# Kernel tuning notes

Measured on AMD Instinct MI355X. Metric: run time of the kernel, lower is better.

Reference implementation:

```python
import jax, jax.numpy as jnp
import numpy as np

N = 256          # batch size
C = 100          # nb_classes
D = 512          # sz_embed
SCALE = 3.0
EPS = 1e-12      # F.normalize eps
M = N * (N - 1) // 2  # number of (i<j) candidate pairs


def l2norm(x):
    # matches F.normalize(p=2, dim=-1) with eps=1e-12
    return x / jnp.maximum(jnp.linalg.norm(x, axis=-1, keepdims=True), EPS)


def dist_block(A, B):
    # squared euclidean distance block of pairwise_distance(cat([A,B]))[0][:len(A), len(A):]
    # (off-diagonal block, so the eye-masking in the original is a no-op; negatives zeroed)
    d = (A * A).sum(-1, keepdims=True) + (B * B).sum(-1)[None, :] - 2.0 * (A @ B.T)
    return jnp.maximum(d, 0.0)


def setup_inputs() -> dict:
    key = jax.random.key(0)
    k1, k2, k3 = jax.random.split(key, 3)
    X = jax.random.normal(k1, (N, D), dtype=jnp.float32)
    proxies = jax.random.normal(k2, (C, D), dtype=jnp.float32) / 8.0
    T = jax.random.randint(k3, (N,), 0, C)
    indices = jnp.arange(N)  # unused by forward, kept for signature fidelity
    return {"X": X, "proxies": proxies, "T": T, "indices": indices}


def reference(X, proxies, T, indices):
    Pn = SCALE * l2norm(proxies)           # (C, D)
    Xn = SCALE * l2norm(X)                 # (N, D)
    IP = Xn @ Pn.T                         # (N, C) inner-product block

    # --- intercls_mixup (method=1, uncertainty-guided lambdas) ---
    # all i<j pairs; same-class pairs are masked out (original skips them in a Python loop)
    i1, i2 = jnp.triu_indices(N, k=1)      # (M,), (M,)
    diff = T[i1] != T[i2]                  # (M,) valid cross-class pairs
    c1, c2 = T[i1], T[i2]

    X1P1 = jnp.clip(IP[i1, c1], -1.0, 1.0)
    X1P2 = jnp.clip(IP[i1, c2], -1.0, 1.0)
    X2P1 = jnp.clip(IP[i2, c1], -1.0, 1.0)
    X2P2 = jnp.clip(IP[i2, c2], -1.0, 1.0)
    lam = jnp.clip((X2P2 - X2P1) / (X2P2 - X2P1 + X1P1 - X1P2), 0.3, 0.7)
    lam = jnp.where(diff, lam, 0.5)        # neutralize masked (same-class) pairs

    virt = lam[:, None] * Xn[i1] + (1.0 - lam[:, None]) * Xn[i2]  # (M, D)
    virt = l2norm(virt)

    # --- proxy-NCA loss over real + virtual samples ---
    Xall = jnp.concatenate([Xn, SCALE * virt], axis=0)            # (N+M, D)
    Dall = dist_block(Xall, Pn)                                   # (N+M, C)
    logsm = jax.nn.log_softmax(-Dall, axis=-1)

    loss_real = -logsm[jnp.arange(N), T]                          # one-hot targets
    lv = logsm[N:]                                                # (M, C)
    rows = jnp.arange(M)
    # virtual soft targets: lam*onehot(c1) + (1-lam)*onehot(c2)
    loss_virt = -(lam * lv[rows, c1] + (1.0 - lam) * lv[rows, c2])

    total = loss_real.sum() + jnp.sum(jnp.where(diff, loss_virt, 0.0))
    count = N + diff.sum()
    return total / count
```

## Files before the change

kernel.cpp:

```cpp
#include <hip/hip_runtime.h>
#include <hip/hip_bf16.h>
#include <math.h>

#define N_ 256
#define C_ 100
#define D_ 512
#define ST 368
#define NTILE 23
#define NWTILE 529
#define LOG2E 1.44269504088896f

typedef __attribute__((ext_vector_type(8))) short short8;
typedef __attribute__((ext_vector_type(4))) float floatx4;

__device__ inline float waveReduceSum(float v) {
    #pragma unroll
    for (int off = 32; off > 0; off >>= 1) v += __shfl_xor(v, off, 64);
    return v;
}
__device__ inline float clip1(float x) { return fminf(fmaxf(x, -1.0f), 1.0f); }

__device__ inline short8 cvt8(float4 a, float4 b) {
    union { __hip_bfloat16 h[8]; short8 s; } u;
    u.h[0] = __float2bfloat16(a.x); u.h[1] = __float2bfloat16(a.y);
    u.h[2] = __float2bfloat16(a.z); u.h[3] = __float2bfloat16(a.w);
    u.h[4] = __float2bfloat16(b.x); u.h[5] = __float2bfloat16(b.y);
    u.h[6] = __float2bfloat16(b.z); u.h[7] = __float2bfloat16(b.w);
    return u.s;
}

__global__ void gemm_kernel(const float* __restrict__ X,
                            const float* __restrict__ P,
                            float* __restrict__ G,
                            float* __restrict__ rn) {
    int wid = blockIdx.x * 4 + (threadIdx.x >> 6);
    if (wid >= NWTILE) return;
    int lane = threadIdx.x & 63;
    int r = lane & 15, quad = lane >> 4;
    int tm = wid / NTILE, tn = wid - tm * NTILE;
    int ra = tm * 16 + r; if (ra >= 356) ra = 0;
    int rb = tn * 16 + r; if (rb >= 356) rb = 0;
    const float* arow = (ra < N_) ? (X + (size_t)ra * D_) : (P + (size_t)(ra - N_) * D_);
    const float* brow = (rb < N_) ? (X + (size_t)rb * D_) : (P + (size_t)(rb - N_) * D_);
    floatx4 acc = {0.0f, 0.0f, 0.0f, 0.0f};
    #pragma unroll
    for (int kc = 0; kc < D_; kc += 32) {
        const float4* ap = (const float4*)(arow + kc + quad * 8);
        const float4* bp = (const float4*)(brow + kc + quad * 8);
        short8 av = cvt8(ap[0], ap[1]);
        short8 bv = cvt8(bp[0], bp[1]);
        acc = __builtin_amdgcn_mfma_f32_16x16x32_bf16(av, bv, acc, 0, 0, 0);
    }
    int row0 = tm * 16 + quad * 4, col = tn * 16 + r;
    #pragma unroll
    for (int i = 0; i < 4; ++i)
        G[(size_t)(row0 + i) * ST + col] = acc[i];
    if (tm == tn && (r >> 2) == quad) {
        float d = acc[r & 3];
        rn[tm * 16 + r] = 3.0f * rsqrtf(fmaxf(d, 1e-24f));
    }
}

__global__ __launch_bounds__(512)
void pair_kernel(const float* __restrict__ G, const float* __restrict__ rn,
                 const int* __restrict__ T, float* __restrict__ out) {
    __shared__ __attribute__((aligned(16))) float XPl[64 * 104];
    __shared__ __attribute__((aligned(16))) float al[104];
    __shared__ __attribute__((aligned(16))) float sps[104];
    __shared__ float gl[256];
    __shared__ float sxs[256];
    __shared__ int   Tl[256];
    __shared__ int   hist[104];
    __shared__ float red[8];

    int t = threadIdx.x;
    int w = t >> 6, lane = t & 63;
    int bh = blockIdx.x;
    int b = bh & 255, h = bh >> 8;
    int base = h * 64 + 1;

    if (t < 104) { hist[t] = 0; sps[t] = (t < C_) ? rn[256 + t] : 0.0f; }
    if (t < 256) { sxs[t] = rn[t]; Tl[t] = T[t]; gl[t] = G[(size_t)b * ST + t]; }
    if (t < C_)  al[t] = G[(size_t)b * ST + 256 + t];
    #pragma unroll
    for (int it = 0; it < 4; ++it) {
        int id = t + 512 * it;
        if (id < 1600) {
            int row = id / 25, c4 = id - row * 25;
            int gr = (b + base + row) & 255;
            *(float4*)&XPl[row * 104 + c4 * 4] =
                *(const float4*)(G + (size_t)gr * ST + 256 + c4 * 4);
        }
    }
    __syncthreads();
    if (t < 256) atomicAdd(&hist[Tl[t]], 1);

    int m = t >> 3, q = t & 7;
    int t1 = Tl[b];
    float s1 = sxs[b];
    float contrib = 0.0f;
    int nit = (h == 0 && m == 0) ? 2 : 1;
    for (int it = 0; it < nit; ++it) {
        bool isdiag = (it == 1);
        int dd = base + m;
        int i2 = isdiag ? b : ((b + dd) & 255);
        int t2 = Tl[i2];
        bool act = isdiag || ((t2 != t1) && (dd < 128 || b < 128));
        if (!act) continue;
        const float* rowB = isdiag ? al : &XPl[m * 104];
        float sc2 = sxs[i2];
        float ip11 = al[t1] * s1 * sps[t1];
        float ip12 = al[t2] * s1 * sps[t2];
        float ip21 = rowB[t1] * sc2 * sps[t1];
        float ip22 = rowB[t2] * sc2 * sps[t2];
        float X1P1 = clip1(ip11), X1P2 = clip1(ip12);
        float X2P1 = clip1(ip21), X2P2 = clip1(ip22);
        float num = X2P2 - X2P1;
        float den = num + X1P1 - X1P2;
        float lam = fminf(fmaxf(num / den, 0.3f), 0.7f);
        if (isdiag) lam = 1.0f;
        float oml = 1.0f - lam;
        float g = gl[i2] * s1 * sc2;
        float wn2 = 9.0f * (lam * lam + oml * oml) + 2.0f * lam * oml * g;
        float ss2 = 6.0f * rsqrtf(fmaxf(wn2, 1e-24f));
        float la = ss2 * lam * s1 * LOG2E, lb = ss2 * oml * sc2 * LOG2E;
        float sm = 0.0f;
        #pragma unroll
        for (int k = 0; k < 4; ++k) {
            int c = q * 4 + 32 * k;
            if (c < C_) {
                float4 a1 = *(const float4*)&al[c];
                float4 a2 = *(const float4*)&rowB[c];
                float4 s4 = *(const float4*)&sps[c];
                sm += exp2f(s4.x * (la * a1.x + lb * a2.x));
                sm += exp2f(s4.y * (la * a1.y + lb * a2.y));
                sm += exp2f(s4.z * (la * a1.z + lb * a2.z));
                sm += exp2f(s4.w * (la * a1.w + lb * a2.w));
            }
        }
        sm += __shfl_xor(sm, 1, 64);
        sm += __shfl_xor(sm, 2, 64);
        sm += __shfl_xor(sm, 4, 64);
        if (q == 0) {
            float LSE = logf(sm);
            float ec1 = ss2 * (lam * ip11 + oml * ip21);
            float ec2 = ss2 * (lam * ip12 + oml * ip22);
            contrib += LSE - lam * ec1 - oml * ec2;
        }
    }
    float rsum = waveReduceSum(contrib);
    if (lane == 0) red[w] = rsum;
    __syncthreads();

    if (w == 0) {
        float same = 0.0f;
        { float n = (float)hist[lane]; same = 0.5f * n * (n - 1.0f); }
        if (lane + 64 < C_) { float n = (float)hist[lane + 64]; same += 0.5f * n * (n - 1.0f); }
        float bs = (lane < 8) ? red[lane] : 0.0f;
        same = waveReduceSum(same);
        bs = waveReduceSum(bs);
        if (lane == 0) atomicAdd(out, bs / (32896.0f - same));
    }
}

extern "C" void kernel_launch(void* const* d_in, const int* in_sizes, int n_in,
                              void* d_out, int out_size, void* d_ws, size_t ws_size,
                              hipStream_t stream) {
    const float* X = (const float*)d_in[0];
    const float* P = (const float*)d_in[1];
    const int*   T = (const int*)d_in[2];
    float* ws = (float*)d_ws;
    float* G  = ws;
    float* rn = ws + 135424;
    float* out = (float*)d_out;

    gemm_kernel<<<133, 256, 0, stream>>>(X, P, G, rn);
    pair_kernel<<<512, 512, 0, stream>>>(G, rn, T, out);
}
```

Baseline: 77.54 us.

## Split GEMM into X·X, X·P, P·P tiles with K-split and transposed IP layout

The gram GEMM now computes only the needed tiles: X·Xᵀ, X·Pᵀ stored in a class-chunk-major float4 layout, and only the diagonal of P·Pᵀ. Each tile's K dimension is split across four waves and reduced through shared memory. The pair kernel uses one 1024-thread block per row b, with 4 lanes per pair reading the inner-product rows straight from global memory instead of staging them in LDS. This removes redundant P·P and X·P tile work, raises GEMM parallelism and drops the LDS staging. In exchange, the pair kernel takes uncoalesced-ish global reads and has wave imbalance because only j>b pairs are active.

```diff
diff --git a/kernel.cpp b/kernel.cpp
--- a/kernel.cpp
+++ b/kernel.cpp
@@ -5,10 +5,11 @@
 #define N_ 256
 #define C_ 100
 #define D_ 512
-#define ST 368
-#define NTILE 23
-#define NWTILE 529
 #define LOG2E 1.44269504088896f
+
+#define WS_GX  0
+#define WS_GTP 65536
+#define WS_RN  91136
 
 typedef __attribute__((ext_vector_type(8))) short short8;
 typedef __attribute__((ext_vector_type(4))) float floatx4;
@@ -29,134 +30,147 @@
     return u.s;
 }
 
-__global__ void gemm_kernel(const float* __restrict__ X,
-                            const float* __restrict__ P,
-                            float* __restrict__ G,
-                            float* __restrict__ rn) {
-    int wid = blockIdx.x * 4 + (threadIdx.x >> 6);
-    if (wid >= NWTILE) return;
-    int lane = threadIdx.x & 63;
+__global__ __launch_bounds__(256)
+void gemm_kernel(const float* __restrict__ X, const float* __restrict__ P,
+                 float* __restrict__ ws) {
+    float* Gx  = ws + WS_GX;
+    float* GTP = ws + WS_GTP;
+    float* rn  = ws + WS_RN;
+    __shared__ floatx4 accl[3][64];
+    int tile = blockIdx.x;
+    int t = threadIdx.x, w = t >> 6, lane = t & 63;
     int r = lane & 15, quad = lane >> 4;
-    int tm = wid / NTILE, tn = wid - tm * NTILE;
-    int ra = tm * 16 + r; if (ra >= 356) ra = 0;
-    int rb = tn * 16 + r; if (rb >= 356) rb = 0;
-    const float* arow = (ra < N_) ? (X + (size_t)ra * D_) : (P + (size_t)(ra - N_) * D_);
-    const float* brow = (rb < N_) ? (X + (size_t)rb * D_) : (P + (size_t)(rb - N_) * D_);
+    const float *arow, *brow;
+    int tm, tn, mode;
+    if (tile < 256) {
+        mode = 0; tm = tile >> 4; tn = tile & 15;
+        arow = X + (size_t)(tm * 16 + r) * D_;
+        brow = X + (size_t)(tn * 16 + r) * D_;
+    } else if (tile < 368) {
+        int u = tile - 256; mode = 1; tm = u / 7; tn = u - tm * 7;
+        int pb = tn * 16 + r; if (pb >= C_) pb = 0;
+        arow = X + (size_t)(tm * 16 + r) * D_;
+        brow = P + (size_t)pb * D_;
+    } else {
+        mode = 2; tm = tile - 368; tn = tm;
+        int pa = tm * 16 + r; if (pa >= C_) pa = 0;
+        arow = P + (size_t)pa * D_;
+        brow = arow;
+    }
     floatx4 acc = {0.0f, 0.0f, 0.0f, 0.0f};
+    int k0 = w * 128;
     #pragma unroll
-    for (int kc = 0; kc < D_; kc += 32) {
-        const float4* ap = (const float4*)(arow + kc + quad * 8);
-        const float4* bp = (const float4*)(brow + kc + quad * 8);
+    for (int kk = 0; kk < 128; kk += 32) {
+        const float4* ap = (const float4*)(arow + k0 + kk + quad * 8);
+        const float4* bp = (const float4*)(brow + k0 + kk + quad * 8);
         short8 av = cvt8(ap[0], ap[1]);
         short8 bv = cvt8(bp[0], bp[1]);
         acc = __builtin_amdgcn_mfma_f32_16x16x32_bf16(av, bv, acc, 0, 0, 0);
     }
-    int row0 = tm * 16 + quad * 4, col = tn * 16 + r;
-    #pragma unroll
-    for (int i = 0; i < 4; ++i)
-        G[(size_t)(row0 + i) * ST + col] = acc[i];
-    if (tm == tn && (r >> 2) == quad) {
-        float d = acc[r & 3];
-        rn[tm * 16 + r] = 3.0f * rsqrtf(fmaxf(d, 1e-24f));
+    if (w) accl[w - 1][lane] = acc;
+    __syncthreads();
+    if (w == 0) {
+        acc += accl[0][lane]; acc += accl[1][lane]; acc += accl[2][lane];
+        if (mode == 0) {
+            int row0 = tm * 16 + quad * 4, col = tn * 16 + r;
+            #pragma unroll
+            for (int i = 0; i < 4; ++i) Gx[(row0 + i) * 256 + col] = acc[i];
+            if (tm == tn && (r >> 2) == quad)
+                rn[tm * 16 + r] = 3.0f * rsqrtf(fmaxf(acc[r & 3], 1e-24f));
+        } else if (mode == 1) {
+            int c = tn * 16 + r;
+            if (c < C_) {
+                int row0 = tm * 16 + quad * 4;
+                #pragma unroll
+                for (int i = 0; i < 4; ++i)
+                    GTP[(c >> 2) * 1024 + (row0 + i) * 4 + (c & 3)] = acc[i];
+            }
+        } else {
+            if ((r >> 2) == quad) {
+                int pr = tm * 16 + r;
+                if (pr < C_) rn[256 + pr] = 3.0f * rsqrtf(fmaxf(acc[r & 3], 1e-24f));
+            }
+        }
     }
 }
 
-__global__ __launch_bounds__(512)
-void pair_kernel(const float* __restrict__ G, const float* __restrict__ rn,
-                 const int* __restrict__ T, float* __restrict__ out) {
-    __shared__ __attribute__((aligned(16))) float XPl[64 * 104];
-    __shared__ __attribute__((aligned(16))) float al[104];
-    __shared__ __attribute__((aligned(16))) float sps[104];
-    __shared__ float gl[256];
-    __shared__ float sxs[256];
-    __shared__ int   Tl[256];
-    __shared__ int   hist[104];
-    __shared__ float red[8];
+__global__ __launch_bounds__(1024)
+void pair_kernel(const float* __restrict__ ws, const int* __restrict__ T,
+                 float* __restrict__ out) {
+    const float* Gx  = ws + WS_GX;
+    const float4* G4 = (const float4*)(ws + WS_GTP);
+    const float* rn  = ws + WS_RN;
+    __shared__ int Tl[256];
+    __shared__ int hist[C_];
+    __shared__ float sxl[256];
+    __shared__ float red[16];
 
-    int t = threadIdx.x;
-    int w = t >> 6, lane = t & 63;
-    int bh = blockIdx.x;
-    int b = bh & 255, h = bh >> 8;
-    int base = h * 64 + 1;
-
-    if (t < 104) { hist[t] = 0; sps[t] = (t < C_) ? rn[256 + t] : 0.0f; }
-    if (t < 256) { sxs[t] = rn[t]; Tl[t] = T[t]; gl[t] = G[(size_t)b * ST + t]; }
-    if (t < C_)  al[t] = G[(size_t)b * ST + 256 + t];
-    #pragma unroll
-    for (int it = 0; it < 4; ++it) {
-        int id = t + 512 * it;
-        if (id < 1600) {
-            int row = id / 25, c4 = id - row * 25;
-            int gr = (b + base + row) & 255;
-            *(float4*)&XPl[row * 104 + c4 * 4] =
-                *(const float4*)(G + (size_t)gr * ST + 256 + c4 * 4);
-        }
-    }
+    int t = threadIdx.x, w = t >> 6, lane = t & 63;
+    int b = blockIdx.x;
+    if (t < 256) { Tl[t] = T[t]; sxl[t] = rn[t]; }
+    if (t < C_) hist[t] = 0;
     __syncthreads();
     if (t < 256) atomicAdd(&hist[Tl[t]], 1);
 
-    int m = t >> 3, q = t & 7;
+    int m = t >> 2, p = t & 3;
     int t1 = Tl[b];
-    float s1 = sxs[b];
+    float s1 = sxl[b];
+    bool diag = (m == b);
+    bool act = diag || ((m > b) && (Tl[m] != t1));
     float contrib = 0.0f;
-    int nit = (h == 0 && m == 0) ? 2 : 1;
-    for (int it = 0; it < nit; ++it) {
-        bool isdiag = (it == 1);
-        int dd = base + m;
-        int i2 = isdiag ? b : ((b + dd) & 255);
-        int t2 = Tl[i2];
-        bool act = isdiag || ((t2 != t1) && (dd < 128 || b < 128));
-        if (!act) continue;
-        const float* rowB = isdiag ? al : &XPl[m * 104];
-        float sc2 = sxs[i2];
-        float ip11 = al[t1] * s1 * sps[t1];
-        float ip12 = al[t2] * s1 * sps[t2];
-        float ip21 = rowB[t1] * sc2 * sps[t1];
-        float ip22 = rowB[t2] * sc2 * sps[t2];
-        float X1P1 = clip1(ip11), X1P2 = clip1(ip12);
-        float X2P1 = clip1(ip21), X2P2 = clip1(ip22);
-        float num = X2P2 - X2P1;
-        float den = num + X1P1 - X1P2;
-        float lam = fminf(fmaxf(num / den, 0.3f), 0.7f);
-        if (isdiag) lam = 1.0f;
-        float oml = 1.0f - lam;
-        float g = gl[i2] * s1 * sc2;
-        float wn2 = 9.0f * (lam * lam + oml * oml) + 2.0f * lam * oml * g;
-        float ss2 = 6.0f * rsqrtf(fmaxf(wn2, 1e-24f));
-        float la = ss2 * lam * s1 * LOG2E, lb = ss2 * oml * sc2 * LOG2E;
-        float sm = 0.0f;
-        #pragma unroll
-        for (int k = 0; k < 4; ++k) {
-            int c = q * 4 + 32 * k;
-            if (c < C_) {
-                float4 a1 = *(const float4*)&al[c];
-                float4 a2 = *(const float4*)&rowB[c];
-                float4 s4 = *(const float4*)&sps[c];
-                sm += exp2f(s4.x * (la * a1.x + lb * a2.x));
-                sm += exp2f(s4.y * (la * a1.y + lb * a2.y));
-                sm += exp2f(s4.z * (la * a1.z + lb * a2.z));
-                sm += exp2f(s4.w * (la * a1.w + lb * a2.w));
+    if (__ballot(act)) {
+        if (act) {
+            int t2 = Tl[m];
+            float sc2 = sxl[m];
+            float sp1 = rn[256 + t1], sp2 = rn[256 + t2];
+            const float* GTPf = (const float*)G4;
+            float ip11 = GTPf[(t1 >> 2) * 1024 + b * 4 + (t1 & 3)] * s1 * sp1;
+            float ip12 = GTPf[(t2 >> 2) * 1024 + b * 4 + (t2 & 3)] * s1 * sp2;
+            float ip21 = GTPf[(t1 >> 2) * 1024 + m * 4 + (t1 & 3)] * sc2 * sp1;
+            float ip22 = GTPf[(t2 >> 2) * 1024 + m * 4 + (t2 & 3)] * sc2 * sp2;
+            float X1P1 = clip1(ip11), X1P2 = clip1(ip12);
+            float X2P1 = clip1(ip21), X2P2 = clip1(ip22);
+            float num = X2P2 - X2P1;
+            float den = num + X1P1 - X1P2;
+            float lam = fminf(fmaxf(num / den, 0.3f), 0.7f);
+            if (diag) lam = 1.0f;
+            float oml = 1.0f - lam;
+            float g = Gx[b * 256 + m] * s1 * sc2;
+            float wn2 = 9.0f * (lam * lam + oml * oml) + 2.0f * lam * oml * g;
+            float ss2 = 6.0f * rsqrtf(fmaxf(wn2, 1e-24f));
+            float la = ss2 * lam * s1 * LOG2E, lb = ss2 * oml * sc2 * LOG2E;
+            float sm = 0.0f;
+            #pragma unroll
+            for (int k = 0; k < 7; ++k) {
+                int q = p + 4 * k;
+                if (q < 25) {
+                    float4 a1 = G4[q * 256 + b];
+                    float4 a2 = G4[q * 256 + m];
+                    const float4 s4 = *(const float4*)(rn + 256 + q * 4);
+                    sm += exp2f(s4.x * (la * a1.x + lb * a2.x));
+                    sm += exp2f(s4.y * (la * a1.y + lb * a2.y));
+                    sm += exp2f(s4.z * (la * a1.z + lb * a2.z));
+                    sm += exp2f(s4.w * (la * a1.w + lb * a2.w));
+                }
             }
-        }
-        sm += __shfl_xor(sm, 1, 64);
-        sm += __shfl_xor(sm, 2, 64);
-        sm += __shfl_xor(sm, 4, 64);
-        if (q == 0) {
-            float LSE = logf(sm);
-            float ec1 = ss2 * (lam * ip11 + oml * ip21);
-            float ec2 = ss2 * (lam * ip12 + oml * ip22);
-            contrib += LSE - lam * ec1 - oml * ec2;
+            sm += __shfl_xor(sm, 1, 64);
+            sm += __shfl_xor(sm, 2, 64);
+            if (p == 0) {
+                float LSE = logf(sm);
+                float ec1 = ss2 * (lam * ip11 + oml * ip21);
+                float ec2 = ss2 * (lam * ip12 + oml * ip22);
+                contrib = LSE - lam * ec1 - oml * ec2;
+            }
         }
     }
     float rsum = waveReduceSum(contrib);
     if (lane == 0) red[w] = rsum;
     __syncthreads();
-
     if (w == 0) {
-        float same = 0.0f;
+        float same;
         { float n = (float)hist[lane]; same = 0.5f * n * (n - 1.0f); }
         if (lane + 64 < C_) { float n = (float)hist[lane + 64]; same += 0.5f * n * (n - 1.0f); }
-        float bs = (lane < 8) ? red[lane] : 0.0f;
+        float bs = (lane < 16) ? red[lane] : 0.0f;
         same = waveReduceSum(same);
         bs = waveReduceSum(bs);
         if (lane == 0) atomicAdd(out, bs / (32896.0f - same));
@@ -170,10 +184,8 @@
     const float* P = (const float*)d_in[1];
     const int*   T = (const int*)d_in[2];
     float* ws = (float*)d_ws;
-    float* G  = ws;
-    float* rn = ws + 135424;
     float* out = (float*)d_out;
 
-    gemm_kernel<<<133, 256, 0, stream>>>(X, P, G, rn);
-    pair_kernel<<<512, 512, 0, stream>>>(G, rn, T, out);
+    gemm_kernel<<<375, 256, 0, stream>>>(X, P, ws);
+    pair_kernel<<<N_, 1024, 0, stream>>>(ws, T, out);
 }
```

Result: faster. 71.52 us (-7.8%).
